# Kernel tuning notes

Hardware: AMD Instinct MI355X
Metric: run time of the kernel (lower is better)

The kernel has to match this reference:

```python
import jax, jax.numpy as jnp
import numpy as np

N_NODES = 200_000
MEM_DIM = 128
MSG_DIM = 128
TIME_DIM = 100
EDGE_DIM = 128
E = 100_000
RAW_DIM = 2 * MEM_DIM + EDGE_DIM + TIME_DIM  # 484


def setup_inputs() -> dict:
    key = jax.random.key(0)
    ks = jax.random.split(key, 10)
    # TimeEncoder init: w = 1/10^linspace(0,9,dim), b = 0 (as in source)
    time_w = jnp.asarray(1.0 / 10 ** np.linspace(0, 9, TIME_DIM), dtype=jnp.float32).reshape(TIME_DIM, 1)
    time_b = jnp.zeros((TIME_DIM,), jnp.float32)
    s = 0.05  # weight scale to keep gates in a sane range
    return {
        "memory": jax.random.normal(ks[0], (N_NODES, MEM_DIM), jnp.float32),
        "last_update": jax.random.uniform(ks[1], (N_NODES,), jnp.float32),
        "timestamps": jax.random.uniform(ks[2], (E,), jnp.float32) + 1.0,
        "edge_features": jax.random.normal(ks[3], (E, EDGE_DIM), jnp.float32),
        "msg_W": jax.random.normal(ks[4], (MSG_DIM, RAW_DIM), jnp.float32) * s,
        "msg_b": jnp.zeros((MSG_DIM,), jnp.float32),
        "gru_W_ih": jax.random.normal(ks[5], (3 * MEM_DIM, MSG_DIM), jnp.float32) * s,
        "gru_W_hh": jax.random.normal(ks[6], (3 * MEM_DIM, MEM_DIM), jnp.float32) * s,
        "gru_b_ih": jnp.zeros((3 * MEM_DIM,), jnp.float32),
        "gru_b_hh": jnp.zeros((3 * MEM_DIM,), jnp.float32),
        "time_w": time_w,
        "time_b": time_b,
        "source_nodes": jax.random.randint(ks[7], (E,), 0, N_NODES, jnp.int64),
        "destination_nodes": jax.random.randint(ks[8], (E,), 0, N_NODES, jnp.int64),
    }


def reference(memory, last_update, timestamps, edge_features, msg_W, msg_b,
              gru_W_ih, gru_W_hh, gru_b_ih, gru_b_hh, time_w, time_b,
              source_nodes, destination_nodes):
    n_nodes = memory.shape[0]
    # gather memory + time encoding (uses pre-update memory, as in source)
    src_mem = memory[source_nodes]                      # [E, M]
    dst_mem = memory[destination_nodes]                 # [E, M]
    dt = timestamps - last_update[source_nodes]         # [E]
    time_feat = jnp.cos(dt[:, None] * time_w[:, 0][None, :] + time_b)  # [E, T]
    raw = jnp.concatenate([src_mem, dst_mem, edge_features, time_feat], axis=1)  # [E, 484]
    msgs = raw @ msg_W.T + msg_b                        # [E, MSG]
    # each message is buffered at both src and dst -> duplicate and segment-mean
    node_ids = jnp.concatenate([source_nodes, destination_nodes])   # [2E]
    msgs2 = jnp.concatenate([msgs, msgs], axis=0)                    # [2E, MSG]
    sums = jax.ops.segment_sum(msgs2, node_ids, num_segments=n_nodes)
    counts = jax.ops.segment_sum(jnp.ones(node_ids.shape, msgs.dtype), node_ids,
                                 num_segments=n_nodes)               # [N]
    agg = sums / jnp.maximum(counts, 1.0)[:, None]                   # mean aggregator
    # batched GRUCell(agg, memory) — identical math to per-node GRUCell calls
    gi = agg @ gru_W_ih.T + gru_b_ih
    gh = memory @ gru_W_hh.T + gru_b_hh
    i_r, i_z, i_n = jnp.split(gi, 3, axis=1)
    h_r, h_z, h_n = jnp.split(gh, 3, axis=1)
    r = jax.nn.sigmoid(i_r + h_r)
    z = jax.nn.sigmoid(i_z + h_z)
    n = jnp.tanh(i_n + r * h_n)
    h_new = (1.0 - z) * n + z * memory
    active = counts > 0
    new_memory = jnp.where(active[:, None], h_new, memory)
    new_last_update = jnp.where(active, timestamps[0], last_update)
    return new_memory, new_last_update
```

## Files before the change

### kernel.cpp

```cpp
#include <hip/hip_runtime.h>
#include <math.h>

#define N_NODES 200000
#define E_EDGES 100000
#define TIME_DIM 100
#define RAW_DIM 484
#define CAP 10
#define OVF_MAX 8192

typedef short  bf16x8 __attribute__((ext_vector_type(8)));
typedef float  f32x4  __attribute__((ext_vector_type(4)));
typedef unsigned int uint;

__device__ __forceinline__ short f2bf(float f) {
    unsigned u = __builtin_bit_cast(unsigned, f);
    u = (u + 0x7FFFu + ((u >> 16) & 1u)) >> 16;
    return (short)u;
}
__device__ __forceinline__ float bf2f(unsigned short u) {
    return __builtin_bit_cast(float, ((unsigned)u) << 16);
}
__device__ __forceinline__ float fsigmoid(float x) {
    return __builtin_amdgcn_rcpf(1.0f + __expf(-x));
}
__device__ __forceinline__ float ftanh(float x) {
    float t = __expf(2.0f * x);
    return 1.0f - 2.0f * __builtin_amdgcn_rcpf(t + 1.0f);
}
__device__ __forceinline__ unsigned cvtpk(float a, float b) {
    unsigned r;
    asm("v_cvt_pk_bf16_f32 %0, %1, %2" : "=v"(r) : "v"(a), "v"(b));
    return r;
}
__device__ __forceinline__ bf16x8 pack8(float4 a, float4 b) {
    uint4 u = {cvtpk(a.x, a.y), cvtpk(a.z, a.w), cvtpk(b.x, b.y), cvtpk(b.z, b.w)};
    return __builtin_bit_cast(bf16x8, u);
}

__global__ __launch_bounds__(256) void tgn_setup(
    const float* __restrict__ Wih, const float* __restrict__ Whh,
    short* __restrict__ wfg,
    const float* __restrict__ msgW, short* __restrict__ wfm,
    const int* __restrict__ src, const int* __restrict__ dst,
    uint* __restrict__ idxv, uint* __restrict__ cnt, uint* __restrict__ ovf)
{
    int b = blockIdx.x;
    int tid = threadIdx.x;
    if (b < 512) {
        int idx = b * 256 + tid;
        int j = idx & 7;
        int l = (idx >> 3) & 63;
        int s = (idx >> 9) & 7;
        int t = idx >> 12;
        int n = t * 16 + (l & 15);
        int k = s * 32 + (l >> 4) * 8 + j;
        int half = k >> 7;
        int kk = k & 127;
        float v;
        if (n < 256) {
            v = half ? Whh[(size_t)n * 128 + kk] : Wih[(size_t)n * 128 + kk];
        } else if (n < 384) {
            v = half ? 0.0f : Wih[(size_t)n * 128 + kk];
        } else {
            v = half ? Whh[(size_t)(n - 128) * 128 + kk] : 0.0f;
        }
        wfg[idx] = f2bf(v);
    } else if (b < 768) {
        int idx = (b - 512) * 256 + tid;
        int j = idx & 7;
        int l = (idx >> 3) & 63;
        int s = (idx >> 9) & 15;
        int t = idx >> 13;
        int n = t * 16 + (l & 15);
        int k = s * 32 + (l >> 4) * 8 + j;
        float v = (k < RAW_DIM) ? msgW[(size_t)n * RAW_DIM + k] : 0.0f;
        wfm[idx] = f2bf(v);
    } else {
        int i = (b - 768) * 256 + tid;
        if (i < E_EDGES) {
            int s = src[i];
            int d = dst[i];
            uint rs = atomicAdd(&cnt[s], 1u);
            if (rs < CAP) {
                idxv[(size_t)s * CAP + rs] = (uint)i;
            } else {
                uint o = atomicAdd(&ovf[0], 1u);
                if (o < OVF_MAX) { ovf[1 + 2 * o] = (uint)s; ovf[2 + 2 * o] = (uint)i; }
            }
            uint rd = atomicAdd(&cnt[d], 1u);
            if (rd < CAP) {
                idxv[(size_t)d * CAP + rd] = (uint)i;
            } else {
                uint o = atomicAdd(&ovf[0], 1u);
                if (o < OVF_MAX) { ovf[1 + 2 * o] = (uint)d; ovf[2 + 2 * o] = (uint)i; }
            }
        }
    }
}

#define MTE 32

__global__ __launch_bounds__(128, 2) void tgn_msg_f32(
    const float* __restrict__ memory,
    const float* __restrict__ last_update,
    const float* __restrict__ timestamps,
    const float* __restrict__ edge_features,
    const float* __restrict__ msg_b,
    const float* __restrict__ time_w,
    const float* __restrict__ time_b,
    const int*   __restrict__ src,
    const int*   __restrict__ dst,
    const short* __restrict__ wfm,
    float* __restrict__ msgf)
{
    const int tid  = threadIdx.x;
    const int wv   = tid >> 6;
    const int l    = tid & 63;
    const int lrow = l & 15;
    const int lkg  = l >> 4;
    const int e0   = blockIdx.x * MTE + wv * 16;
    const int e    = e0 + lrow;

    const int sid = src[e];
    const int did = dst[e];
    const float dt = timestamps[e] - last_update[sid];

    const float* srcm = memory        + (size_t)sid * 128 + lkg * 8;
    const float* dstm = memory        + (size_t)did * 128 + lkg * 8;
    const float* ef   = edge_features + (size_t)e   * 128 + lkg * 8;
    float4 bufS[8], bufD[8], bufE[8];
#pragma unroll
    for (int s = 0; s < 4; ++s) {
        bufS[2 * s]     = *reinterpret_cast<const float4*>(srcm + s * 32);
        bufS[2 * s + 1] = *reinterpret_cast<const float4*>(srcm + s * 32 + 4);
        bufD[2 * s]     = *reinterpret_cast<const float4*>(dstm + s * 32);
        bufD[2 * s + 1] = *reinterpret_cast<const float4*>(dstm + s * 32 + 4);
        bufE[2 * s]     = *reinterpret_cast<const float4*>(ef + s * 32);
        bufE[2 * s + 1] = *reinterpret_cast<const float4*>(ef + s * 32 + 4);
    }

    bf16x8 afr[16];
#pragma unroll
    for (int s = 12; s < 16; ++s) {
        int k0 = s * 32 + lkg * 8;
        float4 lo, hi;
#pragma unroll
        for (int j = 0; j < 8; ++j) {
            int k = k0 + j;
            float v = 0.0f;
            if (k < RAW_DIM) {
                int t = k - 384;
                v = __cosf(fmaf(dt, time_w[t], time_b[t]));
            }
            if (j < 4) (&lo.x)[j] = v; else (&hi.x)[j - 4] = v;
        }
        afr[s] = pack8(lo, hi);
    }

#pragma unroll
    for (int s = 0; s < 4; ++s) {
        afr[s]     = pack8(bufS[2 * s], bufS[2 * s + 1]);
        afr[4 + s] = pack8(bufD[2 * s], bufD[2 * s + 1]);
        afr[8 + s] = pack8(bufE[2 * s], bufE[2 * s + 1]);
    }

    f32x4 acc[8];
#pragma unroll
    for (int t = 0; t < 8; ++t) acc[t] = (f32x4){0.f, 0.f, 0.f, 0.f};

#pragma unroll
    for (int s = 0; s < 16; ++s) {
#pragma unroll
        for (int t = 0; t < 8; ++t) {
            bf16x8 B = *reinterpret_cast<const bf16x8*>(
                &wfm[(size_t)(((t * 16 + s) * 64) + l) * 8]);
            acc[t] = __builtin_amdgcn_mfma_f32_16x16x32_bf16(afr[s], B, acc[t], 0, 0, 0);
        }
    }

#pragma unroll
    for (int r = 0; r < 4; ++r) {
        int erow = e0 + lkg * 4 + r;
        float* orow = msgf + (size_t)erow * 128;
#pragma unroll
        for (int t = 0; t < 8; ++t) {
            int j = t * 16 + lrow;
            orow[j] = acc[t][r] + msg_b[j];
        }
    }
}

#define GNT 32

__global__ __launch_bounds__(256, 4) void tgn_gru_f32(
    const float* __restrict__ memory,
    const float* __restrict__ last_update,
    const float* __restrict__ timestamps,
    const float* __restrict__ b_ih,
    const float* __restrict__ b_hh,
    const short* __restrict__ wfrag,
    const float* __restrict__ msgf,
    const uint*  __restrict__ idxv,
    const uint*  __restrict__ cnt,
    const uint*  __restrict__ ovf,
    float* __restrict__ out)
{
    __shared__ short X[GNT][264];
    __shared__ float cntS[GNT];

    const int tid = threadIdx.x;
    const int n0 = blockIdx.x * GNT;

    const int nloc = tid >> 3;
    const int p    = tid & 7;
    const int node = n0 + nloc;

    const uint c = cnt[node];
    if (p == 0) cntS[nloc] = (float)c;

#pragma unroll
    for (int it = 0; it < 4; ++it) {
        int i = tid + it * 256;
        int m = i >> 5;
        int c4 = (i & 31) * 4;
        float4 mv = *reinterpret_cast<const float4*>(&memory[(size_t)(n0 + m) * 128 + c4]);
        uint2 u = {cvtpk(mv.x, mv.y), cvtpk(mv.z, mv.w)};
        *reinterpret_cast<uint2*>(&X[m][128 + c4]) = u;
    }

    {
        float a[16];
#pragma unroll
        for (int q = 0; q < 16; ++q) a[q] = 0.0f;
        uint cm = (c < CAP) ? c : (uint)CAP;
        for (uint i = 0; i < cm; ++i) {
            uint eid = idxv[(size_t)node * CAP + i];
            const float* row = msgf + (size_t)eid * 128 + p * 16;
            float4 v0 = *reinterpret_cast<const float4*>(row);
            float4 v1 = *reinterpret_cast<const float4*>(row + 4);
            float4 v2 = *reinterpret_cast<const float4*>(row + 8);
            float4 v3 = *reinterpret_cast<const float4*>(row + 12);
            a[0] += v0.x;  a[1] += v0.y;  a[2]  += v0.z;  a[3]  += v0.w;
            a[4] += v1.x;  a[5] += v1.y;  a[6]  += v1.z;  a[7]  += v1.w;
            a[8] += v2.x;  a[9] += v2.y;  a[10] += v2.z;  a[11] += v2.w;
            a[12] += v3.x; a[13] += v3.y; a[14] += v3.z;  a[15] += v3.w;
        }
        if (c > CAP) {
            uint L = ovf[0];
            if (L > OVF_MAX) L = OVF_MAX;
            for (uint i = 0; i < L; ++i) {
                if (ovf[1 + 2 * i] == (uint)node) {
                    uint eid = ovf[2 + 2 * i];
                    const float* row = msgf + (size_t)eid * 128 + p * 16;
                    float4 v0 = *reinterpret_cast<const float4*>(row);
                    float4 v1 = *reinterpret_cast<const float4*>(row + 4);
                    float4 v2 = *reinterpret_cast<const float4*>(row + 8);
                    float4 v3 = *reinterpret_cast<const float4*>(row + 12);
                    a[0] += v0.x;  a[1] += v0.y;  a[2]  += v0.z;  a[3]  += v0.w;
                    a[4] += v1.x;  a[5] += v1.y;  a[6]  += v1.z;  a[7]  += v1.w;
                    a[8] += v2.x;  a[9] += v2.y;  a[10] += v2.z;  a[11] += v2.w;
                    a[12] += v3.x; a[13] += v3.y; a[14] += v3.z;  a[15] += v3.w;
                }
            }
        }
        float inv = (c > 0) ? (1.0f / (float)c) : 0.0f;
#pragma unroll
        for (int q = 0; q < 16; ++q) a[q] *= inv;
        float4 A0 = {a[0], a[1], a[2], a[3]};
        float4 A1 = {a[4], a[5], a[6], a[7]};
        float4 A2 = {a[8], a[9], a[10], a[11]};
        float4 A3 = {a[12], a[13], a[14], a[15]};
        *reinterpret_cast<bf16x8*>(&X[nloc][p * 16])     = pack8(A0, A1);
        *reinterpret_cast<bf16x8*>(&X[nloc][p * 16 + 8]) = pack8(A2, A3);
    }
    __syncthreads();

    const int w    = tid >> 6;
    const int l    = tid & 63;
    const int lrow = l & 15;
    const int lkg  = l >> 4;

    f32x4 acc[4][2][2];
#pragma unroll
    for (int q = 0; q < 4; q++)
#pragma unroll
        for (int jt = 0; jt < 2; jt++)
#pragma unroll
            for (int mt = 0; mt < 2; mt++)
                acc[q][jt][mt] = (f32x4){0.f, 0.f, 0.f, 0.f};

    for (int s = 0; s < 8; ++s) {
        bf16x8 A[2];
#pragma unroll
        for (int mt = 0; mt < 2; ++mt)
            A[mt] = *reinterpret_cast<const bf16x8*>(&X[mt * 16 + lrow][s * 32 + lkg * 8]);
#pragma unroll
        for (int q = 0; q < 4; ++q)
#pragma unroll
            for (int jt = 0; jt < 2; ++jt) {
                int t = q * 8 + w * 2 + jt;
                bf16x8 B = *reinterpret_cast<const bf16x8*>(&wfrag[(size_t)(((t * 8 + s) * 64) + l) * 8]);
#pragma unroll
                for (int mt = 0; mt < 2; ++mt)
                    acc[q][jt][mt] = __builtin_amdgcn_mfma_f32_16x16x32_bf16(
                        A[mt], B, acc[q][jt][mt], 0, 0, 0);
            }
    }

    const float ts0 = timestamps[0];

#pragma unroll
    for (int jt = 0; jt < 2; ++jt) {
        int j = w * 32 + jt * 16 + lrow;
        float br  = b_ih[j]       + b_hh[j];
        float bz  = b_ih[128 + j] + b_hh[128 + j];
        float bin = b_ih[256 + j];
        float bhn = b_hh[256 + j];
#pragma unroll
        for (int mt = 0; mt < 2; ++mt) {
#pragma unroll
            for (int r = 0; r < 4; ++r) {
                int mloc = mt * 16 + lkg * 4 + r;
                int nodew = n0 + mloc;
                float rg  = acc[0][jt][mt][r] + br;
                float zg  = acc[1][jt][mt][r] + bz;
                float ing = acc[2][jt][mt][r] + bin;
                float hng = acc[3][jt][mt][r] + bhn;
                float rr = fsigmoid(rg);
                float zz = fsigmoid(zg);
                float nn = ftanh(ing + rr * hng);
                float mv = bf2f((unsigned short)X[mloc][128 + j]);
                float h  = (1.0f - zz) * nn + zz * mv;
                out[(size_t)nodew * 128 + j] = (cntS[mloc] > 0.0f) ? h : mv;
            }
        }
    }

    if (tid < GNT) {
        int noded = n0 + tid;
        out[(size_t)N_NODES * 128 + noded] = (cntS[tid] > 0.0f) ? ts0 : last_update[noded];
    }
}

__global__ __launch_bounds__(256) void tgn_prep_wmsg(
    const float* __restrict__ msgW, short* __restrict__ wf)
{
    int idx = blockIdx.x * 256 + threadIdx.x;
    int j = idx & 7;
    int l = (idx >> 3) & 63;
    int s = (idx >> 9) & 15;
    int t = idx >> 13;
    int n = t * 16 + (l & 15);
    int k = s * 32 + (l >> 4) * 8 + j;
    float v = (k < RAW_DIM) ? msgW[(size_t)n * RAW_DIM + k] : 0.0f;
    wf[idx] = f2bf(v);
}

__global__ __launch_bounds__(256) void tgn_prep_wgru(
    const float* __restrict__ Wih, const float* __restrict__ Whh,
    short* __restrict__ wf)
{
    int idx = blockIdx.x * 256 + threadIdx.x;
    int j = idx & 7;
    int l = (idx >> 3) & 63;
    int s = (idx >> 9) & 7;
    int t = idx >> 12;
    int n = t * 16 + (l & 15);
    int k = s * 32 + (l >> 4) * 8 + j;
    int half = k >> 7;
    int kk = k & 127;
    float v;
    if (n < 256) {
        v = half ? Whh[(size_t)n * 128 + kk] : Wih[(size_t)n * 128 + kk];
    } else if (n < 384) {
        v = half ? 0.0f : Wih[(size_t)n * 128 + kk];
    } else {
        v = half ? Whh[(size_t)(n - 128) * 128 + kk] : 0.0f;
    }
    wf[idx] = f2bf(v);
}

#define TE 32

__global__ __launch_bounds__(256, 2) void tgn_msg_mfma(
    const float* __restrict__ memory,
    const float* __restrict__ last_update,
    const float* __restrict__ timestamps,
    const float* __restrict__ edge_features,
    const float* __restrict__ msg_b,
    const float* __restrict__ time_w,
    const float* __restrict__ time_b,
    const int*   __restrict__ src,
    const int*   __restrict__ dst,
    const short* __restrict__ wfm,
    float* __restrict__ sums,
    float* __restrict__ counts)
{
    __shared__ short X[TE][520];
    __shared__ int   sid[TE];
    __shared__ int   did[TE];
    __shared__ float dtS[TE];

    const int tid = threadIdx.x;
    const int e0  = blockIdx.x * TE;

    if (tid < TE) {
        int s = src[e0 + tid];
        int d = dst[e0 + tid];
        sid[tid] = s;
        did[tid] = d;
        dtS[tid] = timestamps[e0 + tid] - last_update[s];
        atomicAdd(&counts[s], 1.0f);
        atomicAdd(&counts[d], 1.0f);
    }
    __syncthreads();

    for (int i = tid; i < TE * 128; i += 256) {
        int e = i >> 7;
        int c = (i & 127) * 4;
        float4 v;
        if (c < 128) {
            v = *reinterpret_cast<const float4*>(&memory[(size_t)sid[e] * 128 + c]);
        } else if (c < 256) {
            v = *reinterpret_cast<const float4*>(&memory[(size_t)did[e] * 128 + (c - 128)]);
        } else if (c < 384) {
            v = *reinterpret_cast<const float4*>(&edge_features[(size_t)(e0 + e) * 128 + (c - 256)]);
        } else if (c < 484) {
            float dt = dtS[e];
            int t = c - 384;
            v.x = __cosf(fmaf(dt, time_w[t + 0], time_b[t + 0]));
            v.y = __cosf(fmaf(dt, time_w[t + 1], time_b[t + 1]));
            v.z = __cosf(fmaf(dt, time_w[t + 2], time_b[t + 2]));
            v.w = __cosf(fmaf(dt, time_w[t + 3], time_b[t + 3]));
        } else {
            v.x = v.y = v.z = v.w = 0.0f;
        }
        short4 s4;
        s4.x = f2bf(v.x); s4.y = f2bf(v.y); s4.z = f2bf(v.z); s4.w = f2bf(v.w);
        *reinterpret_cast<short4*>(&X[e][c]) = s4;
    }
    __syncthreads();

    const int w    = tid >> 6;
    const int l    = tid & 63;
    const int lrow = l & 15;
    const int lkg  = l >> 4;
    const int et   = w & 1;
    const int nh   = w >> 1;

    f32x4 acc[4];
#pragma unroll
    for (int n = 0; n < 4; n++) acc[n] = (f32x4){0.f, 0.f, 0.f, 0.f};

#pragma unroll 4
    for (int s = 0; s < 16; ++s) {
        bf16x8 A = *reinterpret_cast<const bf16x8*>(&X[et * 16 + lrow][s * 32 + lkg * 8]);
#pragma unroll
        for (int ntl = 0; ntl < 4; ++ntl) {
            int t = nh * 4 + ntl;
            bf16x8 B = *reinterpret_cast<const bf16x8*>(&wfm[(size_t)(((t * 16 + s) * 64) + l) * 8]);
            acc[ntl] = __builtin_amdgcn_mfma_f32_16x16x32_bf16(A, B, acc[ntl], 0, 0, 0);
        }
    }

#pragma unroll
    for (int ntl = 0; ntl < 4; ++ntl) {
        int j = nh * 64 + ntl * 16 + lrow;
        float bias = msg_b[j];
#pragma unroll
        for (int r = 0; r < 4; ++r) {
            int el = et * 16 + lkg * 4 + r;
            float m = acc[ntl][r] + bias;
            atomicAdd(&sums[(size_t)sid[el] * 128 + j], m);
            atomicAdd(&sums[(size_t)did[el] * 128 + j], m);
        }
    }
}

__global__ __launch_bounds__(256, 3) void tgn_gru_mfma(
    const float* __restrict__ memory,
    const float* __restrict__ last_update,
    const float* __restrict__ timestamps,
    const float* __restrict__ b_ih,
    const float* __restrict__ b_hh,
    const short* __restrict__ wfrag,
    float* __restrict__ out)
{
    __shared__ short X[GNT][264];
    __shared__ float cntS[GNT];

    const int tid = threadIdx.x;
    const int n0 = blockIdx.x * GNT;
    const float* sums   = out;
    const float* counts = out + (size_t)N_NODES * 128;

    if (tid < GNT) cntS[tid] = counts[n0 + tid];
    __syncthreads();

    for (int i = tid; i < GNT * 32; i += 256) {
        int m = i >> 5;
        int c = (i & 31) * 4;
        float inv = 1.0f / fmaxf(cntS[m], 1.0f);
        float4 v = *reinterpret_cast<const float4*>(&sums[(size_t)(n0 + m) * 128 + c]);
        short4 a4;
        a4.x = f2bf(v.x * inv); a4.y = f2bf(v.y * inv);
        a4.z = f2bf(v.z * inv); a4.w = f2bf(v.w * inv);
        *reinterpret_cast<short4*>(&X[m][c]) = a4;
        float4 mv = *reinterpret_cast<const float4*>(&memory[(size_t)(n0 + m) * 128 + c]);
        short4 m4;
        m4.x = f2bf(mv.x); m4.y = f2bf(mv.y); m4.z = f2bf(mv.z); m4.w = f2bf(mv.w);
        *reinterpret_cast<short4*>(&X[m][128 + c]) = m4;
    }
    __syncthreads();

    const int w    = tid >> 6;
    const int l    = tid & 63;
    const int lrow = l & 15;
    const int lkg  = l >> 4;

    f32x4 acc[4][2][2];
#pragma unroll
    for (int q = 0; q < 4; q++)
#pragma unroll
        for (int jt = 0; jt < 2; jt++)
#pragma unroll
            for (int mt = 0; mt < 2; mt++)
                acc[q][jt][mt] = (f32x4){0.f, 0.f, 0.f, 0.f};

    for (int s = 0; s < 8; ++s) {
        bf16x8 A[2];
#pragma unroll
        for (int mt = 0; mt < 2; ++mt)
            A[mt] = *reinterpret_cast<const bf16x8*>(&X[mt * 16 + lrow][s * 32 + lkg * 8]);
#pragma unroll
        for (int q = 0; q < 4; ++q)
#pragma unroll
            for (int jt = 0; jt < 2; ++jt) {
                int t = q * 8 + w * 2 + jt;
                bf16x8 B = *reinterpret_cast<const bf16x8*>(&wfrag[(size_t)(((t * 8 + s) * 64) + l) * 8]);
#pragma unroll
                for (int mt = 0; mt < 2; ++mt)
                    acc[q][jt][mt] = __builtin_amdgcn_mfma_f32_16x16x32_bf16(
                        A[mt], B, acc[q][jt][mt], 0, 0, 0);
            }
    }

    const float ts0 = timestamps[0];
#pragma unroll
    for (int jt = 0; jt < 2; ++jt) {
        int j = w * 32 + jt * 16 + lrow;
        float br  = b_ih[j]       + b_hh[j];
        float bz  = b_ih[128 + j] + b_hh[128 + j];
        float bin = b_ih[256 + j];
        float bhn = b_hh[256 + j];
#pragma unroll
        for (int mt = 0; mt < 2; ++mt) {
#pragma unroll
            for (int r = 0; r < 4; ++r) {
                int mloc = mt * 16 + lkg * 4 + r;
                int node = n0 + mloc;
                float rg  = acc[0][jt][mt][r] + br;
                float zg  = acc[1][jt][mt][r] + bz;
                float ing = acc[2][jt][mt][r] + bin;
                float hng = acc[3][jt][mt][r] + bhn;
                float rr = fsigmoid(rg);
                float zz = fsigmoid(zg);
                float nn = ftanh(ing + rr * hng);
                float mv = memory[(size_t)node * 128 + j];
                float h  = (1.0f - zz) * nn + zz * mv;
                out[(size_t)node * 128 + j] = (cntS[mloc] > 0.0f) ? h : mv;
            }
        }
    }
    if (tid < GNT) {
        int node = n0 + tid;
        out[(size_t)N_NODES * 128 + node] = (cntS[tid] > 0.0f) ? ts0 : last_update[node];
    }
}

extern "C" void kernel_launch(void* const* d_in, const int* in_sizes, int n_in,
                              void* d_out, int out_size, void* d_ws, size_t ws_size,
                              hipStream_t stream) {
    const float* memory        = (const float*)d_in[0];
    const float* last_update   = (const float*)d_in[1];
    const float* timestamps    = (const float*)d_in[2];
    const float* edge_features = (const float*)d_in[3];
    const float* msg_W         = (const float*)d_in[4];
    const float* msg_b         = (const float*)d_in[5];
    const float* gru_W_ih      = (const float*)d_in[6];
    const float* gru_W_hh      = (const float*)d_in[7];
    const float* gru_b_ih      = (const float*)d_in[8];
    const float* gru_b_hh      = (const float*)d_in[9];
    const float* time_w        = (const float*)d_in[10];
    const float* time_b        = (const float*)d_in[11];
    const int*   src           = (const int*)d_in[12];
    const int*   dst           = (const int*)d_in[13];

    float* out = (float*)d_out;
    char* ws = (char*)d_ws;

    const size_t OFF_WGRU = 0;
    const size_t OFF_WMSG = 262144;
    const size_t OFF_MSGF = 393216;
    const size_t SZ_MSGF  = (size_t)E_EDGES * 128 * 4;
    const size_t OFF_IDX  = OFF_MSGF + SZ_MSGF;
    const size_t SZ_IDX   = (size_t)N_NODES * CAP * 4;
    const size_t OFF_CNT  = OFF_IDX + SZ_IDX;
    const size_t OFF_OVF  = OFF_CNT + (size_t)N_NODES * 4;
    const size_t WS_NEED  = OFF_OVF + 4 + (size_t)OVF_MAX * 8;

    short* wfrag_gru = (short*)(ws + OFF_WGRU);
    short* wfrag_msg = (short*)(ws + OFF_WMSG);

    if (ws_size >= WS_NEED) {
        float* msgf = (float*)(ws + OFF_MSGF);
        uint*  idxv = (uint*)(ws + OFF_IDX);
        uint*  cnt  = (uint*)(ws + OFF_CNT);
        uint*  ovf  = (uint*)(ws + OFF_OVF);

        hipMemsetAsync(ws + OFF_CNT, 0, (size_t)N_NODES * 4 + 16, stream);

        const int TICKET_BLOCKS = (E_EDGES + 255) / 256;
        tgn_setup<<<768 + TICKET_BLOCKS, 256, 0, stream>>>(
            gru_W_ih, gru_W_hh, wfrag_gru, msg_W, wfrag_msg,
            src, dst, idxv, cnt, ovf);

        tgn_msg_f32<<<E_EDGES / MTE, 128, 0, stream>>>(
            memory, last_update, timestamps, edge_features, msg_b,
            time_w, time_b, src, dst, wfrag_msg, msgf);

        tgn_gru_f32<<<N_NODES / GNT, 256, 0, stream>>>(
            memory, last_update, timestamps, gru_b_ih, gru_b_hh, wfrag_gru,
            msgf, idxv, cnt, ovf, out);
    } else {
        hipMemsetAsync(d_out, 0, (size_t)out_size * sizeof(float), stream);
        float* sums   = out;
        float* counts = out + (size_t)N_NODES * 128;

        tgn_prep_wgru<<<512, 256, 0, stream>>>(gru_W_ih, gru_W_hh, wfrag_gru);
        tgn_prep_wmsg<<<256, 256, 0, stream>>>(msg_W, wfrag_msg);

        tgn_msg_mfma<<<E_EDGES / TE, 256, 0, stream>>>(
            memory, last_update, timestamps, edge_features, msg_b,
            time_w, time_b, src, dst, wfrag_msg, sums, counts);

        tgn_gru_mfma<<<N_NODES / GNT, 256, 0, stream>>>(
            memory, last_update, timestamps, gru_b_ih, gru_b_hh, wfrag_gru, out);
    }
}
```

Before: 242.7 us.

## Compact active nodes so GRU GEMM runs only on touched nodes

The setup kernel now appends each node to a compacted active list on its first atomic ticket. A new GRU kernel runs the MFMA GEMM only over blocks of active nodes, and extra blocks copy memory and last_update through for inactive nodes. The per-node index capacity grows to 12 so the index lists can be read as uint4 loads with an unrolled gather. This avoids GEMM and gather work for the roughly half of nodes with no messages, at the cost of an extra atomic counter, a scattered output write pattern, and a grid sized for the worst case.

```diff
diff --git a/kernel.cpp b/kernel.cpp
--- a/kernel.cpp
+++ b/kernel.cpp
@@ -5,8 +5,8 @@
 #define E_EDGES 100000
 #define TIME_DIM 100
 #define RAW_DIM 484
-#define CAP 10
 #define OVF_MAX 8192
+#define INVALID_NODE 0xFFFFFFFFu
 
 typedef short  bf16x8 __attribute__((ext_vector_type(8)));
 typedef float  f32x4  __attribute__((ext_vector_type(4)));
@@ -37,12 +37,14 @@
     return __builtin_bit_cast(bf16x8, u);
 }
 
+template<int CAPX, bool ACT>
 __global__ __launch_bounds__(256) void tgn_setup(
     const float* __restrict__ Wih, const float* __restrict__ Whh,
     short* __restrict__ wfg,
     const float* __restrict__ msgW, short* __restrict__ wfm,
     const int* __restrict__ src, const int* __restrict__ dst,
-    uint* __restrict__ idxv, uint* __restrict__ cnt, uint* __restrict__ ovf)
+    uint* __restrict__ idxv, uint* __restrict__ cnt, uint* __restrict__ ovf,
+    uint* __restrict__ nact, uint* __restrict__ activev)
 {
     int b = blockIdx.x;
     int tid = threadIdx.x;
@@ -81,15 +83,23 @@
             int s = src[i];
             int d = dst[i];
             uint rs = atomicAdd(&cnt[s], 1u);
-            if (rs < CAP) {
-                idxv[(size_t)s * CAP + rs] = (uint)i;
+            if (ACT && rs == 0u) {
+                uint ppos = atomicAdd(nact, 1u);
+                activev[ppos] = (uint)s;
+            }
+            if (rs < (uint)CAPX) {
+                idxv[(size_t)s * CAPX + rs] = (uint)i;
             } else {
                 uint o = atomicAdd(&ovf[0], 1u);
                 if (o < OVF_MAX) { ovf[1 + 2 * o] = (uint)s; ovf[2 + 2 * o] = (uint)i; }
             }
             uint rd = atomicAdd(&cnt[d], 1u);
-            if (rd < CAP) {
-                idxv[(size_t)d * CAP + rd] = (uint)i;
+            if (ACT && rd == 0u) {
+                uint ppos = atomicAdd(nact, 1u);
+                activev[ppos] = (uint)d;
+            }
+            if (rd < (uint)CAPX) {
+                idxv[(size_t)d * CAPX + rd] = (uint)i;
             } else {
                 uint o = atomicAdd(&ovf[0], 1u);
                 if (o < OVF_MAX) { ovf[1 + 2 * o] = (uint)d; ovf[2 + 2 * o] = (uint)i; }
@@ -191,7 +201,209 @@
 }
 
 #define GNT 32
-
+#define GRID_GEMM ((N_NODES + GNT - 1) / GNT)
+#define COPY_EXTRA 64
+
+__global__ __launch_bounds__(256, 4) void tgn_gru_act(
+    const float* __restrict__ memory,
+    const float* __restrict__ last_update,
+    const float* __restrict__ timestamps,
+    const float* __restrict__ b_ih,
+    const float* __restrict__ b_hh,
+    const short* __restrict__ wfrag,
+    const float* __restrict__ msgf,
+    const uint*  __restrict__ idxv,
+    const uint*  __restrict__ cnt,
+    const uint*  __restrict__ ovf,
+    const uint*  __restrict__ nactv,
+    const uint*  __restrict__ activev,
+    float* __restrict__ out)
+{
+    __shared__ short X[GNT][264];
+    __shared__ float cntS[GNT];
+    __shared__ uint  anS[GNT];
+
+    const int tid = threadIdx.x;
+    const uint nact = nactv[0];
+    const uint nab  = (nact + GNT - 1) / GNT;
+    const int  bid  = blockIdx.x;
+
+    if (bid >= (int)nab) {
+        const uint ncb = (uint)gridDim.x - nab;
+        const uint cb  = (uint)bid - nab;
+        const uint lo = (uint)(((unsigned long long)N_NODES * cb) / ncb);
+        const uint hi = (uint)(((unsigned long long)N_NODES * (cb + 1)) / ncb);
+        const int  sub = tid & 31;
+        for (uint base = lo; base < hi; base += 8) {
+            uint node = base + (uint)(tid >> 5);
+            if (node < hi && cnt[node] == 0u) {
+                int c4 = sub * 4;
+                *reinterpret_cast<float4*>(&out[(size_t)node * 128 + c4]) =
+                    *reinterpret_cast<const float4*>(&memory[(size_t)node * 128 + c4]);
+                if (sub == 0)
+                    out[(size_t)N_NODES * 128 + node] = last_update[node];
+            }
+        }
+        return;
+    }
+
+    const int n0 = bid * GNT;
+    if (tid < GNT) {
+        uint a = ((uint)(n0 + tid) < nact) ? activev[n0 + tid] : INVALID_NODE;
+        anS[tid] = a;
+    }
+    __syncthreads();
+
+    const int  nloc  = tid >> 3;
+    const int  p     = tid & 7;
+    const uint anode = anS[nloc];
+    const bool valid = (anode != INVALID_NODE);
+    const uint c     = valid ? cnt[anode] : 0u;
+    if (p == 0) cntS[nloc] = (float)c;
+
+#pragma unroll
+    for (int it = 0; it < 4; ++it) {
+        int i = tid + it * 256;
+        int m = i >> 5;
+        int c4 = (i & 31) * 4;
+        uint an = anS[m];
+        uint rn = (an == INVALID_NODE) ? 0u : an;
+        float4 mv = *reinterpret_cast<const float4*>(&memory[(size_t)rn * 128 + c4]);
+        uint2 u = {cvtpk(mv.x, mv.y), cvtpk(mv.z, mv.w)};
+        *reinterpret_cast<uint2*>(&X[m][128 + c4]) = u;
+    }
+
+    {
+        float a[16];
+#pragma unroll
+        for (int q = 0; q < 16; ++q) a[q] = 0.0f;
+        const uint cm = (c < 12u) ? c : 12u;
+        if (cm > 0u) {
+            const uint* ip = idxv + (size_t)anode * 12;
+            uint4 i0 = *reinterpret_cast<const uint4*>(ip);
+            uint4 i1 = {0, 0, 0, 0}, i2 = {0, 0, 0, 0};
+            if (cm > 4u) i1 = *reinterpret_cast<const uint4*>(ip + 4);
+            if (cm > 8u) i2 = *reinterpret_cast<const uint4*>(ip + 8);
+            uint idxs[12];
+            idxs[0] = i0.x; idxs[1] = i0.y; idxs[2]  = i0.z; idxs[3]  = i0.w;
+            idxs[4] = i1.x; idxs[5] = i1.y; idxs[6]  = i1.z; idxs[7]  = i1.w;
+            idxs[8] = i2.x; idxs[9] = i2.y; idxs[10] = i2.z; idxs[11] = i2.w;
+#pragma unroll
+            for (int i = 0; i < 12; ++i) {
+                if ((uint)i < cm) {
+                    const float* row = msgf + (size_t)idxs[i] * 128 + p * 16;
+                    float4 v0 = *reinterpret_cast<const float4*>(row);
+                    float4 v1 = *reinterpret_cast<const float4*>(row + 4);
+                    float4 v2 = *reinterpret_cast<const float4*>(row + 8);
+                    float4 v3 = *reinterpret_cast<const float4*>(row + 12);
+                    a[0] += v0.x;  a[1] += v0.y;  a[2]  += v0.z;  a[3]  += v0.w;
+                    a[4] += v1.x;  a[5] += v1.y;  a[6]  += v1.z;  a[7]  += v1.w;
+                    a[8] += v2.x;  a[9] += v2.y;  a[10] += v2.z;  a[11] += v2.w;
+                    a[12] += v3.x; a[13] += v3.y; a[14] += v3.z;  a[15] += v3.w;
+                }
+            }
+        }
+        if (c > 12u) {
+            uint L = ovf[0];
+            if (L > OVF_MAX) L = OVF_MAX;
+            for (uint i = 0; i < L; ++i) {
+                if (ovf[1 + 2 * i] == anode) {
+                    uint eid = ovf[2 + 2 * i];
+                    const float* row = msgf + (size_t)eid * 128 + p * 16;
+                    float4 v0 = *reinterpret_cast<const float4*>(row);
+                    float4 v1 = *reinterpret_cast<const float4*>(row + 4);
+                    float4 v2 = *reinterpret_cast<const float4*>(row + 8);
+                    float4 v3 = *reinterpret_cast<const float4*>(row + 12);
+                    a[0] += v0.x;  a[1] += v0.y;  a[2]  += v0.z;  a[3]  += v0.w;
+                    a[4] += v1.x;  a[5] += v1.y;  a[6]  += v1.z;  a[7]  += v1.w;
+                    a[8] += v2.x;  a[9] += v2.y;  a[10] += v2.z;  a[11] += v2.w;
+                    a[12] += v3.x; a[13] += v3.y; a[14] += v3.z;  a[15] += v3.w;
+                }
+            }
+        }
+        float inv = (c > 0u) ? (1.0f / (float)c) : 0.0f;
+#pragma unroll
+        for (int q = 0; q < 16; ++q) a[q] *= inv;
+        float4 A0 = {a[0], a[1], a[2], a[3]};
+        float4 A1 = {a[4], a[5], a[6], a[7]};
+        float4 A2 = {a[8], a[9], a[10], a[11]};
+        float4 A3 = {a[12], a[13], a[14], a[15]};
+        *reinterpret_cast<bf16x8*>(&X[nloc][p * 16])     = pack8(A0, A1);
+        *reinterpret_cast<bf16x8*>(&X[nloc][p * 16 + 8]) = pack8(A2, A3);
+    }
+    __syncthreads();
+
+    const int w    = tid >> 6;
+    const int l    = tid & 63;
+    const int lrow = l & 15;
+    const int lkg  = l >> 4;
+
+    f32x4 acc[4][2][2];
+#pragma unroll
+    for (int q = 0; q < 4; q++)
+#pragma unroll
+        for (int jt = 0; jt < 2; jt++)
+#pragma unroll
+            for (int mt = 0; mt < 2; mt++)
+                acc[q][jt][mt] = (f32x4){0.f, 0.f, 0.f, 0.f};
+
+    for (int s = 0; s < 8; ++s) {
+        bf16x8 A[2];
+#pragma unroll
+        for (int mt = 0; mt < 2; ++mt)
+            A[mt] = *reinterpret_cast<const bf16x8*>(&X[mt * 16 + lrow][s * 32 + lkg * 8]);
+#pragma unroll
+        for (int q = 0; q < 4; ++q)
+#pragma unroll
+            for (int jt = 0; jt < 2; ++jt) {
+                int t = q * 8 + w * 2 + jt;
+                bf16x8 B = *reinterpret_cast<const bf16x8*>(&wfrag[(size_t)(((t * 8 + s) * 64) + l) * 8]);
+#pragma unroll
+                for (int mt = 0; mt < 2; ++mt)
+                    acc[q][jt][mt] = __builtin_amdgcn_mfma_f32_16x16x32_bf16(
+                        A[mt], B, acc[q][jt][mt], 0, 0, 0);
+            }
+    }
+
+    const float ts0 = timestamps[0];
+
+#pragma unroll
+    for (int jt = 0; jt < 2; ++jt) {
+        int j = w * 32 + jt * 16 + lrow;
+        float br  = b_ih[j]       + b_hh[j];
+        float bz  = b_ih[128 + j] + b_hh[128 + j];
+        float bin = b_ih[256 + j];
+        float bhn = b_hh[256 + j];
+#pragma unroll
+        for (int mt = 0; mt < 2; ++mt) {
+#pragma unroll
+            for (int r = 0; r < 4; ++r) {
+                int mloc = mt * 16 + lkg * 4 + r;
+                uint an = anS[mloc];
+                if (an != INVALID_NODE) {
+                    float rg  = acc[0][jt][mt][r] + br;
+                    float zg  = acc[1][jt][mt][r] + bz;
+                    float ing = acc[2][jt][mt][r] + bin;
+                    float hng = acc[3][jt][mt][r] + bhn;
+                    float rr = fsigmoid(rg);
+                    float zz = fsigmoid(zg);
+                    float nn = ftanh(ing + rr * hng);
+                    float mv = bf2f((unsigned short)X[mloc][128 + j]);
+                    float h  = (1.0f - zz) * nn + zz * mv;
+                    out[(size_t)an * 128 + j] = h;
+                }
+            }
+        }
+    }
+
+    if (tid < GNT) {
+        uint an = anS[tid];
+        if (an != INVALID_NODE)
+            out[(size_t)N_NODES * 128 + an] = ts0;
+    }
+}
+
+template<int CAPX>
 __global__ __launch_bounds__(256, 4) void tgn_gru_f32(
     const float* __restrict__ memory,
     const float* __restrict__ last_update,
@@ -232,9 +444,9 @@
         float a[16];
 #pragma unroll
         for (int q = 0; q < 16; ++q) a[q] = 0.0f;
-        uint cm = (c < CAP) ? c : (uint)CAP;
+        uint cm = (c < (uint)CAPX) ? c : (uint)CAPX;
         for (uint i = 0; i < cm; ++i) {
-            uint eid = idxv[(size_t)node * CAP + i];
+            uint eid = idxv[(size_t)node * CAPX + i];
             const float* row = msgf + (size_t)eid * 128 + p * 16;
             float4 v0 = *reinterpret_cast<const float4*>(row);
             float4 v1 = *reinterpret_cast<const float4*>(row + 4);
@@ -245,7 +457,7 @@
             a[8] += v2.x;  a[9] += v2.y;  a[10] += v2.z;  a[11] += v2.w;
             a[12] += v3.x; a[13] += v3.y; a[14] += v3.z;  a[15] += v3.w;
         }
-        if (c > CAP) {
+        if (c > (uint)CAPX) {
             uint L = ovf[0];
             if (L > OVF_MAX) L = OVF_MAX;
             for (uint i = 0; i < L; ++i) {
@@ -340,44 +552,6 @@
         int noded = n0 + tid;
         out[(size_t)N_NODES * 128 + noded] = (cntS[tid] > 0.0f) ? ts0 : last_update[noded];
     }
-}
-
-__global__ __launch_bounds__(256) void tgn_prep_wmsg(
-    const float* __restrict__ msgW, short* __restrict__ wf)
-{
-    int idx = blockIdx.x * 256 + threadIdx.x;
-    int j = idx & 7;
-    int l = (idx >> 3) & 63;
-    int s = (idx >> 9) & 15;
-    int t = idx >> 13;
-    int n = t * 16 + (l & 15);
-    int k = s * 32 + (l >> 4) * 8 + j;
-    float v = (k < RAW_DIM) ? msgW[(size_t)n * RAW_DIM + k] : 0.0f;
-    wf[idx] = f2bf(v);
-}
-
-__global__ __launch_bounds__(256) void tgn_prep_wgru(
-    const float* __restrict__ Wih, const float* __restrict__ Whh,
-    short* __restrict__ wf)
-{
-    int idx = blockIdx.x * 256 + threadIdx.x;
-    int j = idx & 7;
-    int l = (idx >> 3) & 63;
-    int s = (idx >> 9) & 7;
-    int t = idx >> 12;
-    int n = t * 16 + (l & 15);
-    int k = s * 32 + (l >> 4) * 8 + j;
-    int half = k >> 7;
-    int kk = k & 127;
-    float v;
-    if (n < 256) {
-        v = half ? Whh[(size_t)n * 128 + kk] : Wih[(size_t)n * 128 + kk];
-    } else if (n < 384) {
-        v = half ? 0.0f : Wih[(size_t)n * 128 + kk];
-    } else {
-        v = half ? Whh[(size_t)(n - 128) * 128 + kk] : 0.0f;
-    }
-    wf[idx] = f2bf(v);
 }
 
 #define TE 32
@@ -603,33 +777,63 @@
     const size_t OFF_WMSG = 262144;
     const size_t OFF_MSGF = 393216;
     const size_t SZ_MSGF  = (size_t)E_EDGES * 128 * 4;
-    const size_t OFF_IDX  = OFF_MSGF + SZ_MSGF;
-    const size_t SZ_IDX   = (size_t)N_NODES * CAP * 4;
-    const size_t OFF_CNT  = OFF_IDX + SZ_IDX;
-    const size_t OFF_OVF  = OFF_CNT + (size_t)N_NODES * 4;
-    const size_t WS_NEED  = OFF_OVF + 4 + (size_t)OVF_MAX * 8;
+
+    const size_t OFF_IDX1 = OFF_MSGF + SZ_MSGF;
+    const size_t SZ_IDX1  = (size_t)N_NODES * 12 * 4;
+    const size_t OFF_CNT1 = OFF_IDX1 + SZ_IDX1;
+    const size_t OFF_NACT = OFF_CNT1 + (size_t)N_NODES * 4;
+    const size_t OFF_OVF1 = OFF_NACT + 16;
+    const size_t OFF_ACT  = OFF_OVF1 + 4 + (size_t)OVF_MAX * 8;
+    const size_t WS1      = OFF_ACT + (size_t)N_NODES * 4;
+
+    const size_t OFF_IDX2 = OFF_MSGF + SZ_MSGF;
+    const size_t SZ_IDX2  = (size_t)N_NODES * 10 * 4;
+    const size_t OFF_CNT2 = OFF_IDX2 + SZ_IDX2;
+    const size_t OFF_OVF2 = OFF_CNT2 + (size_t)N_NODES * 4;
+    const size_t WS2      = OFF_OVF2 + 4 + (size_t)OVF_MAX * 8;
 
     short* wfrag_gru = (short*)(ws + OFF_WGRU);
     short* wfrag_msg = (short*)(ws + OFF_WMSG);
-
-    if (ws_size >= WS_NEED) {
-        float* msgf = (float*)(ws + OFF_MSGF);
-        uint*  idxv = (uint*)(ws + OFF_IDX);
-        uint*  cnt  = (uint*)(ws + OFF_CNT);
-        uint*  ovf  = (uint*)(ws + OFF_OVF);
-
-        hipMemsetAsync(ws + OFF_CNT, 0, (size_t)N_NODES * 4 + 16, stream);
-
-        const int TICKET_BLOCKS = (E_EDGES + 255) / 256;
-        tgn_setup<<<768 + TICKET_BLOCKS, 256, 0, stream>>>(
+    const int TICKET_BLOCKS = (E_EDGES + 255) / 256;
+
+    if (ws_size >= WS1) {
+        float* msgf  = (float*)(ws + OFF_MSGF);
+        uint*  idxv  = (uint*)(ws + OFF_IDX1);
+        uint*  cnt   = (uint*)(ws + OFF_CNT1);
+        uint*  nactv = (uint*)(ws + OFF_NACT);
+        uint*  ovf   = (uint*)(ws + OFF_OVF1);
+        uint*  actv  = (uint*)(ws + OFF_ACT);
+
+        hipMemsetAsync(ws + OFF_CNT1, 0, (size_t)N_NODES * 4 + 20, stream);
+
+        tgn_setup<12, true><<<768 + TICKET_BLOCKS, 256, 0, stream>>>(
             gru_W_ih, gru_W_hh, wfrag_gru, msg_W, wfrag_msg,
-            src, dst, idxv, cnt, ovf);
+            src, dst, idxv, cnt, ovf, nactv, actv);
 
         tgn_msg_f32<<<E_EDGES / MTE, 128, 0, stream>>>(
             memory, last_update, timestamps, edge_features, msg_b,
             time_w, time_b, src, dst, wfrag_msg, msgf);
 
-        tgn_gru_f32<<<N_NODES / GNT, 256, 0, stream>>>(
+        tgn_gru_act<<<GRID_GEMM + COPY_EXTRA, 256, 0, stream>>>(
+            memory, last_update, timestamps, gru_b_ih, gru_b_hh, wfrag_gru,
+            msgf, idxv, cnt, ovf, nactv, actv, out);
+    } else if (ws_size >= WS2) {
+        float* msgf = (float*)(ws + OFF_MSGF);
+        uint*  idxv = (uint*)(ws + OFF_IDX2);
+        uint*  cnt  = (uint*)(ws + OFF_CNT2);
+        uint*  ovf  = (uint*)(ws + OFF_OVF2);
+
+        hipMemsetAsync(ws + OFF_CNT2, 0, (size_t)N_NODES * 4 + 16, stream);
+
+        tgn_setup<10, false><<<768 + TICKET_BLOCKS, 256, 0, stream>>>(
+            gru_W_ih, gru_W_hh, wfrag_gru, msg_W, wfrag_msg,
+            src, dst, idxv, cnt, ovf, nullptr, nullptr);
+
+        tgn_msg_f32<<<E_EDGES / MTE, 128, 0, stream>>>(
+            memory, last_update, timestamps, edge_features, msg_b,
+            time_w, time_b, src, dst, wfrag_msg, msgf);
+
+        tgn_gru_f32<10><<<N_NODES / GNT, 256, 0, stream>>>(
             memory, last_update, timestamps, gru_b_ih, gru_b_hh, wfrag_gru,
             msgf, idxv, cnt, ovf, out);
     } else {
@@ -637,8 +841,9 @@
         float* sums   = out;
         float* counts = out + (size_t)N_NODES * 128;
 
-        tgn_prep_wgru<<<512, 256, 0, stream>>>(gru_W_ih, gru_W_hh, wfrag_gru);
-        tgn_prep_wmsg<<<256, 256, 0, stream>>>(msg_W, wfrag_msg);
+        tgn_setup<10, false><<<768, 256, 0, stream>>>(
+            gru_W_ih, gru_W_hh, wfrag_gru, msg_W, wfrag_msg,
+            src, dst, nullptr, nullptr, nullptr, nullptr, nullptr);
 
         tgn_msg_mfma<<<E_EDGES / TE, 256, 0, stream>>>(
             memory, last_update, timestamps, edge_features, msg_b,
```

Result: slower. 278.5 us (+14.7%).
